# Performance work log

Hardware: AMD Instinct MI355X
Metric: run time of the kernel (lower is better)

Reference implementation:

```python
import jax, jax.numpy as jnp
import numpy as np

B, T, LD, HD, NH, NL = 8, 16, 256, 512, 8, 6
N = 65           # num_patches + 1 tokens per frame from encoder
AED = 64         # action_embed_dim
NDA = 11         # num_discrete_actions
MLP = 4 * HD


def _ln(x, g, b, eps=1e-5):
    m = jnp.mean(x, -1, keepdims=True)
    v = jnp.mean((x - m) ** 2, -1, keepdims=True)
    return (x - m) / jnp.sqrt(v + eps) * g + b


def setup_inputs() -> dict:
    key = jax.random.key(0)
    ks = iter(jax.random.split(key, 48))
    def nrm(shape):
        return jax.random.normal(next(ks), shape, jnp.float32) * 0.02
    inp = {
        'z_sequence': jax.random.normal(next(ks), (B, T, N, LD), jnp.float32),
        'continuous_actions': jax.random.normal(next(ks), (B, T, 2), jnp.float32),
        'discrete_actions': jax.random.randint(next(ks), (B, T), 0, NDA),
        'w_de': nrm((NDA, AED)),
        'w_cp': nrm((2, AED)), 'b_cp': jnp.zeros((AED,), jnp.float32),
        'w_ap': nrm((2 * AED, HD)), 'b_ap': jnp.zeros((HD,), jnp.float32),
        'w_tp': nrm((LD, HD)), 'b_tp': jnp.zeros((HD,), jnp.float32),
        'w_te': nrm((64, HD)),
        'ln1_g': jnp.ones((NL, HD), jnp.float32), 'ln1_b': jnp.zeros((NL, HD), jnp.float32),
        'wq': nrm((NL, HD, HD)), 'bq': jnp.zeros((NL, HD), jnp.float32),
        'wk': nrm((NL, HD, HD)), 'bk': jnp.zeros((NL, HD), jnp.float32),
        'wv': nrm((NL, HD, HD)), 'bv': jnp.zeros((NL, HD), jnp.float32),
        'wo': nrm((NL, HD, HD)), 'bo': jnp.zeros((NL, HD), jnp.float32),
        'ln2_g': jnp.ones((NL, HD), jnp.float32), 'ln2_b': jnp.zeros((NL, HD), jnp.float32),
        'w1': nrm((NL, HD, MLP)), 'b1': jnp.zeros((NL, MLP), jnp.float32),
        'w2': nrm((NL, MLP, HD)), 'b2': jnp.zeros((NL, HD), jnp.float32),
        'norm_g': jnp.ones((HD,), jnp.float32), 'norm_b': jnp.zeros((HD,), jnp.float32),
        'w_out': nrm((HD, LD)), 'b_out': jnp.zeros((LD,), jnp.float32),
        'residual_weight': jnp.float32(0.5),
    }
    return inp


def reference(z_sequence, continuous_actions, discrete_actions,
              w_de, w_cp, b_cp, w_ap, b_ap, w_tp, b_tp, w_te,
              ln1_g, ln1_b, wq, bq, wk, bk, wv, bv, wo, bo,
              ln2_g, ln2_b, w1, b1, w2, b2,
              norm_g, norm_b, w_out, b_out, residual_weight):
    Bq, Tq, Nq, Dq = z_sequence.shape
    hd = HD // NH
    scale = hd ** -0.5
    # --- per-timestep action + patch token embedding (vectorized over T) ---
    de = w_de[discrete_actions]                          # (B,T,AED)
    ce = continuous_actions @ w_cp + b_cp                # (B,T,AED)
    ac = jnp.concatenate([de, ce], -1)                   # (B,T,2*AED)
    at = (ac @ w_ap + b_ap)[:, :, None, :]               # (B,T,1,HD) action token
    pt = z_sequence @ w_tp + b_tp                        # (B,T,N,HD)
    te = w_te[:Tq][None, :, None, :]                     # (1,T,1,HD) time embedding
    x = jnp.concatenate([at + te, pt + te], axis=2)      # (B,T,1+N,HD) interleaved
    S = Tq * (Nq + 1)
    x = x.reshape(Bq, S, HD)
    # --- block-causal mask: True = cannot attend ---
    ts = jnp.repeat(jnp.arange(Tq), Nq + 1)
    mask = ts[None, :] > ts[:, None]                     # (S,S)

    def body(h, p):
        g1, be1, Wq, Bq_, Wk, Bk_, Wv, Bv_, Wo, Bo_, g2, be2, W1, B1, W2, B2 = p
        y = _ln(h, g1, be1)
        q = (y @ Wq + Bq_).reshape(Bq, S, NH, hd)
        k = (y @ Wk + Bk_).reshape(Bq, S, NH, hd)
        v = (y @ Wv + Bv_).reshape(Bq, S, NH, hd)
        sc = jnp.einsum('bqhd,bkhd->bhqk', q, k) * scale
        sc = jnp.where(mask[None, None], -jnp.inf, sc)
        a = jax.nn.softmax(sc, axis=-1)
        o = jnp.einsum('bhqk,bkhd->bqhd', a, v).reshape(Bq, S, HD)
        h = h + o @ Wo + Bo_
        y = _ln(h, g2, be2)
        h = h + jax.nn.gelu(y @ W1 + B1, approximate=False) @ W2 + B2
        return h, None

    x, _ = jax.lax.scan(body, x, (ln1_g, ln1_b, wq, bq, wk, bk, wv, bv, wo, bo,
                                  ln2_g, ln2_b, w1, b1, w2, b2))
    x = _ln(x, norm_g, norm_b)
    patch_out = x.reshape(Bq, Tq, Nq + 1, HD)[:, :, 1:, :] @ w_out + b_out
    alpha = jax.nn.sigmoid(residual_weight)
    return z_sequence + alpha * patch_out
```

## Files before the change

kernel.cpp:

```cpp
#include <hip/hip_runtime.h>
#include <hip/hip_bf16.h>
#include <cmath>

typedef __attribute__((ext_vector_type(8)))  __bf16 bf16x8;
typedef __attribute__((ext_vector_type(4)))  float  f32x4;
typedef __attribute__((ext_vector_type(16))) float  f32x16;
typedef const __attribute__((address_space(1))) void* as1cv;
typedef __attribute__((address_space(3))) void*       as3v;

#define GBAR()  asm volatile("s_barrier" ::: "memory")
#define VMW0()  asm volatile("s_waitcnt vmcnt(0)" ::: "memory")

static constexpr int BB = 8, TT = 16, NN = 65, LD = 256, HD = 512, NH = 8, NL = 6;
static constexpr int SS    = TT * (NN + 1);
static constexpr int ROWS  = BB * SS;
static constexpr int PROWS = BB * TT * NN;
static constexpr int MLPD  = 2048;

__global__ void transpose_cast(const float* __restrict__ in, __bf16* __restrict__ out,
                               int R, int C, size_t ibs, size_t obs)
{
  __shared__ float t[32][33];
  in  += ibs * blockIdx.z;
  out += obs * blockIdx.z;
  int bx = blockIdx.x * 32, by = blockIdx.y * 32;
  #pragma unroll
  for (int i = threadIdx.y; i < 32; i += 8)
    t[i][threadIdx.x] = in[(size_t)(by + i) * C + bx + threadIdx.x];
  __syncthreads();
  #pragma unroll
  for (int i = threadIdx.y; i < 32; i += 8)
    out[(size_t)(bx + i) * R + by + threadIdx.x] = (__bf16)t[threadIdx.x][i];
}

__global__ __launch_bounds__(256) void cast_bf16(const float* __restrict__ in,
                                                 __bf16* __restrict__ out)
{
  int i = (blockIdx.x * 256 + threadIdx.x) * 8;
  float4 a = *(const float4*)(in + i);
  float4 b = *(const float4*)(in + i + 4);
  bf16x8 o;
  o[0]=(__bf16)a.x; o[1]=(__bf16)a.y; o[2]=(__bf16)a.z; o[3]=(__bf16)a.w;
  o[4]=(__bf16)b.x; o[5]=(__bf16)b.y; o[6]=(__bf16)b.z; o[7]=(__bf16)b.w;
  *(bf16x8*)(out + i) = o;
}

__global__ void build_bqkv(const float* __restrict__ bq, const float* __restrict__ bk,
                           const float* __restrict__ bv, float* __restrict__ out)
{
  int i = blockIdx.x * 256 + threadIdx.x;
  int L = i / 1536, c = i % 1536;
  float v = (c < 512) ? bq[L*512 + c] : (c < 1024 ? bk[L*512 + c - 512] : bv[L*512 + c - 1024]);
  out[i] = v;
}

template<int FLAGS>
__global__ __launch_bounds__(256)
void gemm_bt(const __bf16* __restrict__ A, const __bf16* __restrict__ Bt,
             const float* __restrict__ bias, const float* __restrict__ resid,
             float* __restrict__ outF, __bf16* __restrict__ outB, __bf16* __restrict__ outB2,
             int M, int N, int K)
{
  __shared__ __bf16 As[64 * 64];
  __shared__ __bf16 Bs[128 * 64];
  const int tid = threadIdx.x;
  const int lane = tid & 63, w = tid >> 6;
  const int g = lane >> 4, cl = lane & 15;
  const int wr = w >> 1, wc = w & 1;
  const int gx = gridDim.x, nwg = gx * gridDim.y;
  const int orig = blockIdx.y * gx + blockIdx.x;
  const int q8 = nwg >> 3, r8 = nwg & 7;
  const int xcd = orig & 7, off = orig >> 3;
  const int tile = (xcd < r8 ? xcd * (q8 + 1) : r8 * (q8 + 1) + (xcd - r8) * q8) + off;
  const int tm = (tile / gx) * 64, tn = (tile % gx) * 128;

  f32x4 acc[2][4];
  const f32x4 zero4 = {0.f, 0.f, 0.f, 0.f};
  #pragma unroll
  for (int m = 0; m < 2; m++)
    #pragma unroll
    for (int n = 0; n < 4; n++) acc[m][n] = zero4;

  const int nk = K >> 6;
  for (int kt = 0; kt < nk; ++kt) {
    __syncthreads();
    const __bf16* Ag = A  + (size_t)tm * K + kt * 64;
    const __bf16* Bg = Bt + (size_t)tn * K + kt * 64;
    #pragma unroll
    for (int p = 0; p < 2; p++) {
      int c = p * 256 + tid;
      int row = c >> 3, j = c & 7;
      int jj = j ^ (row & 7);
      const __bf16* sa = Ag + (size_t)row * K + jj * 8;
      __builtin_amdgcn_global_load_lds((as1cv)sa, (as3v)&As[(p * 4 + w) * 512], 16, 0, 0);
    }
    #pragma unroll
    for (int p = 0; p < 4; p++) {
      int c = p * 256 + tid;
      int row = c >> 3, j = c & 7;
      int jj = j ^ (row & 7);
      const __bf16* sb = Bg + (size_t)row * K + jj * 8;
      __builtin_amdgcn_global_load_lds((as1cv)sb, (as3v)&Bs[(p * 4 + w) * 512], 16, 0, 0);
    }
    __syncthreads();
    #pragma unroll
    for (int kk = 0; kk < 2; kk++) {
      bf16x8 af[2], bfr[4];
      #pragma unroll
      for (int m = 0; m < 2; m++) {
        int row = wr * 32 + m * 16 + cl;
        af[m] = *(const bf16x8*)&As[row * 64 + ((kk * 4 + g) ^ (row & 7)) * 8];
      }
      #pragma unroll
      for (int n = 0; n < 4; n++) {
        int row = wc * 64 + n * 16 + cl;
        bfr[n] = *(const bf16x8*)&Bs[row * 64 + ((kk * 4 + g) ^ (row & 7)) * 8];
      }
      #pragma unroll
      for (int m = 0; m < 2; m++)
        #pragma unroll
        for (int n = 0; n < 4; n++)
          acc[m][n] = __builtin_amdgcn_mfma_f32_16x16x32_bf16(af[m], bfr[n], acc[m][n], 0, 0, 0);
    }
  }
  float bv[4];
  #pragma unroll
  for (int n = 0; n < 4; n++) bv[n] = bias[tn + wc * 64 + n * 16 + cl];
  #pragma unroll
  for (int m = 0; m < 2; m++) {
    int Rb = tm + wr * 32 + m * 16 + g * 4;
    #pragma unroll
    for (int i = 0; i < 4; i++) {
      int R = Rb + i;
      #pragma unroll
      for (int n = 0; n < 4; n++) {
        int C = tn + wc * 64 + n * 16 + cl;
        float v = acc[m][n][i] + bv[n];
        if (FLAGS & 1) v = 0.5f * v * (1.f + erff(v * 0.70710678118f));
        if (FLAGS & 2) v += resid[(size_t)R * N + C];
        if (FLAGS & 8) outF[(size_t)R * N + C] = v;
        if (FLAGS & 4) outB[(size_t)R * N + C] = (__bf16)v;
        if (FLAGS & 32) {
          if (C < 1024) {
            outB[(size_t)R * 1024 + C] = (__bf16)v;
          } else {
            int bb2 = R / SS, s2 = R % SS;
            int cc = C - 1024, hh = cc >> 6, dd = cc & 63;
            outB2[((size_t)((bb2 * NH + hh) * 64 + dd)) * SS + s2] = (__bf16)v;
          }
        }
      }
    }
  }
}

__global__ __launch_bounds__(256) void ln_bf16(const float* __restrict__ in,
    const float* __restrict__ gam, const float* __restrict__ bet, __bf16* __restrict__ out)
{
  int w = threadIdx.x >> 6, l = threadIdx.x & 63;
  size_t row = (size_t)blockIdx.x * 4 + w;
  const float4* x4 = (const float4*)(in + row * HD);
  float4 v0 = x4[l], v1 = x4[l + 64];
  float s  = v0.x + v0.y + v0.z + v0.w + v1.x + v1.y + v1.z + v1.w;
  float q2 = v0.x*v0.x + v0.y*v0.y + v0.z*v0.z + v0.w*v0.w
           + v1.x*v1.x + v1.y*v1.y + v1.z*v1.z + v1.w*v1.w;
  #pragma unroll
  for (int m = 1; m < 64; m <<= 1) { s += __shfl_xor(s, m); q2 += __shfl_xor(q2, m); }
  float mean = s * (1.f / HD);
  float rstd = rsqrtf(q2 * (1.f / HD) - mean * mean + 1e-5f);
  int c0 = l * 4, c1 = 256 + l * 4;
  float4 g0 = *(const float4*)(gam + c0), g1 = *(const float4*)(gam + c1);
  float4 e0 = *(const float4*)(bet + c0), e1 = *(const float4*)(bet + c1);
  __bf16* o = out + row * HD;
  o[c0+0] = (__bf16)((v0.x-mean)*rstd*g0.x + e0.x);
  o[c0+1] = (__bf16)((v0.y-mean)*rstd*g0.y + e0.y);
  o[c0+2] = (__bf16)((v0.z-mean)*rstd*g0.z + e0.z);
  o[c0+3] = (__bf16)((v0.w-mean)*rstd*g0.w + e0.w);
  o[c1+0] = (__bf16)((v1.x-mean)*rstd*g1.x + e1.x);
  o[c1+1] = (__bf16)((v1.y-mean)*rstd*g1.y + e1.y);
  o[c1+2] = (__bf16)((v1.z-mean)*rstd*g1.z + e1.z);
  o[c1+3] = (__bf16)((v1.w-mean)*rstd*g1.w + e1.w);
}

__global__ __launch_bounds__(64) void act_embed(const float* __restrict__ cont,
    const int* __restrict__ disc, const float* __restrict__ w_de,
    const float* __restrict__ w_cp, const float* __restrict__ b_cp,
    const float* __restrict__ w_ap, const float* __restrict__ b_ap,
    const float* __restrict__ w_te, float* __restrict__ x)
{
  int t = blockIdx.x, b = blockIdx.y, l = threadIdx.x;
  int da = disc[b * TT + t];
  float c0 = cont[(b * TT + t) * 2], c1 = cont[(b * TT + t) * 2 + 1];
  int c = l * 8;
  float accv[8];
  #pragma unroll
  for (int j = 0; j < 8; j++) accv[j] = b_ap[c + j];
  for (int i = 0; i < 64; i++) {
    float ai = w_de[da * 64 + i];
    #pragma unroll
    for (int j = 0; j < 8; j++) accv[j] += ai * w_ap[i * HD + c + j];
  }
  for (int i = 0; i < 64; i++) {
    float ce = c0 * w_cp[i] + c1 * w_cp[64 + i] + b_cp[i];
    #pragma unroll
    for (int j = 0; j < 8; j++) accv[j] += ce * w_ap[(64 + i) * HD + c + j];
  }
  #pragma unroll
  for (int j = 0; j < 8; j++)
    x[((size_t)(b * SS) + t * 66) * HD + c + j] = accv[j] + w_te[t * HD + c + j];
}

__global__ __launch_bounds__(256) void assemble_patch(const float* __restrict__ pt,
    const float* __restrict__ te, float* __restrict__ x)
{
  int idx = (blockIdx.x * 256 + threadIdx.x) * 4;
  int c = idx & (HD - 1);
  int r = idx >> 9;
  int n = r % NN; int bt = r / NN; int t = bt & (TT - 1); int bb = bt >> 4;
  float4 v  = *(const float4*)(pt + idx);
  float4 tv = *(const float4*)(te + t * HD + c);
  v.x += tv.x; v.y += tv.y; v.z += tv.z; v.w += tv.w;
  *(float4*)(x + ((size_t)(bb * SS + t * 66 + 1 + n)) * HD + c) = v;
}

__device__ inline unsigned pkbf(float lo, float hi2) {
  unsigned short a = __builtin_bit_cast(unsigned short, (__bf16)lo);
  unsigned short b = __builtin_bit_cast(unsigned short, (__bf16)hi2);
  return (unsigned)a | ((unsigned)b << 16);
}

__global__ __launch_bounds__(256) void attn_fwd(const __bf16* __restrict__ qk,
    const __bf16* __restrict__ vT, __bf16* __restrict__ o)
{
  const int tid = threadIdx.x;
  const int w = tid >> 6, lane = tid & 63;
  const int h = blockIdx.y, b = blockIdx.z;
  const int l31 = lane & 31, hi = lane >> 5;
  const int qt = blockIdx.x * 4 + w;
  const bool qv = qt <= 32;
  const int q = qv ? qt * 32 + l31 : 0;
  const int kend = (q / 66 + 1) * 66;

  __shared__ __attribute__((aligned(16))) __bf16 Ks[2][64][64];
  __shared__ __attribute__((aligned(16))) __bf16 Vs[2][64][64];
  __shared__ float red[4][32];

  const int qtmax = min(blockIdx.x * 4 + 3, 32);
  const int nkv_b = (((qtmax * 32 + 31) / 66 + 1) * 66 + 63) >> 6;
  const int nkv_w = qv ? ((((qt * 32 + 31) / 66 + 1) * 66 + 63) >> 6) : 0;

  bf16x8 qf[4];
  const __bf16* qbase = qk + (size_t)(b * SS + q) * 1024 + h * 64 + hi * 8;
  #pragma unroll
  for (int s = 0; s < 4; s++) qf[s] = *(const bf16x8*)(qbase + s * 16);

  const f32x16 z16 = {0,0,0,0,0,0,0,0,0,0,0,0,0,0,0,0};
  f32x16 accA = z16, accB = z16;
  float m = -1e30f, lsum = 0.f;

  auto stage = [&](int buf, int kb) {
    const int K0 = kb * 64;
    #pragma unroll
    for (int p2 = 0; p2 < 2; p2++) {
      int c = p2 * 256 + tid;
      int row = c >> 3, j = c & 7;
      int jj = j ^ (row & 7);
      const __bf16* sk = qk + (size_t)(b * SS + min(K0 + row, SS - 1)) * 1024 + 512
                            + h * 64 + jj * 8;
      __builtin_amdgcn_global_load_lds((as1cv)sk,
          (as3v)(&Ks[buf][0][0] + (p2 * 4 + w) * 512), 16, 0, 0);
      const __bf16* sv = vT + (size_t)((b * NH + h) * 64 + row) * SS
                            + min(K0 + jj * 8, SS - 8);
      __builtin_amdgcn_global_load_lds((as1cv)sv,
          (as3v)(&Vs[buf][0][0] + (p2 * 4 + w) * 512), 16, 0, 0);
    }
  };

  stage(0, 0);
  VMW0();
  GBAR();

  int buf = 0;
  for (int kb = 0; kb < nkv_b; ++kb) {
    if (kb + 1 < nkv_b) stage(buf ^ 1, kb + 1);
    if (qv && kb < nkv_w) {
      const int K0 = kb * 64;
      bf16x8 kfa[4], kfb[4], vfa[4], vfb[4];
      #pragma unroll
      for (int s = 0; s < 4; s++) {
        int ch = ((s * 2 + hi) ^ (l31 & 7)) * 8;
        kfa[s] = *(const bf16x8*)&Ks[buf][l31][ch];
        kfb[s] = *(const bf16x8*)&Ks[buf][32 + l31][ch];
        vfa[s] = *(const bf16x8*)&Vs[buf][l31][ch];
        vfb[s] = *(const bf16x8*)&Vs[buf][32 + l31][ch];
      }
      f32x16 st0 = z16, st1 = z16;
      st0 = __builtin_amdgcn_mfma_f32_32x32x16_bf16(kfa[0], qf[0], st0, 0, 0, 0);
      st0 = __builtin_amdgcn_mfma_f32_32x32x16_bf16(kfa[1], qf[1], st0, 0, 0, 0);
      st0 = __builtin_amdgcn_mfma_f32_32x32x16_bf16(kfa[2], qf[2], st0, 0, 0, 0);
      st0 = __builtin_amdgcn_mfma_f32_32x32x16_bf16(kfa[3], qf[3], st0, 0, 0, 0);
      st1 = __builtin_amdgcn_mfma_f32_32x32x16_bf16(kfb[0], qf[0], st1, 0, 0, 0);
      st1 = __builtin_amdgcn_mfma_f32_32x32x16_bf16(kfb[1], qf[1], st1, 0, 0, 0);
      st1 = __builtin_amdgcn_mfma_f32_32x32x16_bf16(kfb[2], qf[2], st1, 0, 0, 0);
      st1 = __builtin_amdgcn_mfma_f32_32x32x16_bf16(kfb[3], qf[3], st1, 0, 0, 0);

      float p0[16], p1[16];
      #pragma unroll
      for (int r = 0; r < 16; r++) {
        int cr = (r & 3) + 8 * (r >> 2) + 4 * hi;
        p0[r] = (K0 + cr < kend)      ? st0[r] * 0.125f : -1e30f;
        p1[r] = (K0 + 32 + cr < kend) ? st1[r] * 0.125f : -1e30f;
      }
      float mx = fmaxf(fmaxf(fmaxf(p0[0],p0[1]),fmaxf(p0[2],p0[3])),
                       fmaxf(fmaxf(p0[4],p0[5]),fmaxf(p0[6],p0[7])));
      mx = fmaxf(mx, fmaxf(fmaxf(fmaxf(p0[8],p0[9]),fmaxf(p0[10],p0[11])),
                           fmaxf(fmaxf(p0[12],p0[13]),fmaxf(p0[14],p0[15]))));
      mx = fmaxf(mx, fmaxf(fmaxf(fmaxf(p1[0],p1[1]),fmaxf(p1[2],p1[3])),
                           fmaxf(fmaxf(p1[4],p1[5]),fmaxf(p1[6],p1[7]))));
      mx = fmaxf(mx, fmaxf(fmaxf(fmaxf(p1[8],p1[9]),fmaxf(p1[10],p1[11])),
                           fmaxf(fmaxf(p1[12],p1[13]),fmaxf(p1[14],p1[15]))));
      mx = fmaxf(mx, __shfl_xor(mx, 32));
      if (__any(mx > m + 8.f)) {
        float nm = fmaxf(m, mx);
        float alp = __expf(m - nm);
        m = nm; lsum *= alp;
        if (lane < 32) red[w][lane] = alp;
        asm volatile("s_waitcnt lgkmcnt(0)" ::: "memory");
        float4 a0 = *(const float4*)&red[w][hi * 4];
        float4 a1 = *(const float4*)&red[w][hi * 4 + 8];
        float4 a2 = *(const float4*)&red[w][hi * 4 + 16];
        float4 a3 = *(const float4*)&red[w][hi * 4 + 24];
        float afv[16] = {a0.x,a0.y,a0.z,a0.w, a1.x,a1.y,a1.z,a1.w,
                         a2.x,a2.y,a2.z,a2.w, a3.x,a3.y,a3.z,a3.w};
        #pragma unroll
        for (int r = 0; r < 16; r++) { accA[r] *= afv[r]; accB[r] *= afv[r]; }
      }
      #pragma unroll
      for (int r = 0; r < 16; r++) { p0[r] = __expf(p0[r] - m); p1[r] = __expf(p1[r] - m); }
      float rs = (((p0[0]+p0[1])+(p0[2]+p0[3])) + ((p0[4]+p0[5])+(p0[6]+p0[7])))
               + (((p0[8]+p0[9])+(p0[10]+p0[11])) + ((p0[12]+p0[13])+(p0[14]+p0[15])))
               + (((p1[0]+p1[1])+(p1[2]+p1[3])) + ((p1[4]+p1[5])+(p1[6]+p1[7])))
               + (((p1[8]+p1[9])+(p1[10]+p1[11])) + ((p1[12]+p1[13])+(p1[14]+p1[15])));
      rs += __shfl_xor(rs, 32);
      lsum += rs;
      union { unsigned u[4]; bf16x8 v; } af00, af10, af01, af11;
      {
        unsigned a0p = pkbf(p0[0], p0[1]),  a1p = pkbf(p0[2], p0[3]);
        unsigned a2p = pkbf(p0[4], p0[5]),  a3p = pkbf(p0[6], p0[7]);
        unsigned b0p = pkbf(p0[8], p0[9]),  b1p = pkbf(p0[10], p0[11]);
        unsigned b2p = pkbf(p0[12], p0[13]), b3p = pkbf(p0[14], p0[15]);
        unsigned s0 = __shfl_xor(a0p, 32), s1 = __shfl_xor(a1p, 32);
        unsigned s2 = __shfl_xor(a2p, 32), s3 = __shfl_xor(a3p, 32);
        unsigned t0 = __shfl_xor(b0p, 32), t1 = __shfl_xor(b1p, 32);
        unsigned t2 = __shfl_xor(b2p, 32), t3 = __shfl_xor(b3p, 32);
        af00.u[0] = hi ? s2 : a0p;  af00.u[1] = hi ? s3 : a1p;
        af00.u[2] = hi ? a2p : s0;  af00.u[3] = hi ? a3p : s1;
        af10.u[0] = hi ? t2 : b0p;  af10.u[1] = hi ? t3 : b1p;
        af10.u[2] = hi ? b2p : t0;  af10.u[3] = hi ? b3p : t1;
      }
      {
        unsigned a0p = pkbf(p1[0], p1[1]),  a1p = pkbf(p1[2], p1[3]);
        unsigned a2p = pkbf(p1[4], p1[5]),  a3p = pkbf(p1[6], p1[7]);
        unsigned b0p = pkbf(p1[8], p1[9]),  b1p = pkbf(p1[10], p1[11]);
        unsigned b2p = pkbf(p1[12], p1[13]), b3p = pkbf(p1[14], p1[15]);
        unsigned s0 = __shfl_xor(a0p, 32), s1 = __shfl_xor(a1p, 32);
        unsigned s2 = __shfl_xor(a2p, 32), s3 = __shfl_xor(a3p, 32);
        unsigned t0 = __shfl_xor(b0p, 32), t1 = __shfl_xor(b1p, 32);
        unsigned t2 = __shfl_xor(b2p, 32), t3 = __shfl_xor(b3p, 32);
        af01.u[0] = hi ? s2 : a0p;  af01.u[1] = hi ? s3 : a1p;
        af01.u[2] = hi ? a2p : s0;  af01.u[3] = hi ? a3p : s1;
        af11.u[0] = hi ? t2 : b0p;  af11.u[1] = hi ? t3 : b1p;
        af11.u[2] = hi ? b2p : t0;  af11.u[3] = hi ? b3p : t1;
      }
      accA = __builtin_amdgcn_mfma_f32_32x32x16_bf16(af00.v, vfa[0], accA, 0, 0, 0);
      accA = __builtin_amdgcn_mfma_f32_32x32x16_bf16(af10.v, vfa[1], accA, 0, 0, 0);
      accA = __builtin_amdgcn_mfma_f32_32x32x16_bf16(af01.v, vfa[2], accA, 0, 0, 0);
      accA = __builtin_amdgcn_mfma_f32_32x32x16_bf16(af11.v, vfa[3], accA, 0, 0, 0);
      accB = __builtin_amdgcn_mfma_f32_32x32x16_bf16(af00.v, vfb[0], accB, 0, 0, 0);
      accB = __builtin_amdgcn_mfma_f32_32x32x16_bf16(af10.v, vfb[1], accB, 0, 0, 0);
      accB = __builtin_amdgcn_mfma_f32_32x32x16_bf16(af01.v, vfb[2], accB, 0, 0, 0);
      accB = __builtin_amdgcn_mfma_f32_32x32x16_bf16(af11.v, vfb[3], accB, 0, 0, 0);
    }
    VMW0();
    GBAR();
    buf ^= 1;
  }

  if (qv) {
    if (lane < 32) red[w][lane] = 1.f / lsum;
    asm volatile("s_waitcnt lgkmcnt(0)" ::: "memory");
    float4 i0 = *(const float4*)&red[w][hi * 4];
    float4 i1 = *(const float4*)&red[w][hi * 4 + 8];
    float4 i2 = *(const float4*)&red[w][hi * 4 + 16];
    float4 i3 = *(const float4*)&red[w][hi * 4 + 24];
    float iv[16] = {i0.x,i0.y,i0.z,i0.w, i1.x,i1.y,i1.z,i1.w,
                    i2.x,i2.y,i2.z,i2.w, i3.x,i3.y,i3.z,i3.w};
    __bf16* obase = o + (size_t)(b * SS + qt * 32) * HD + h * 64 + l31;
    #pragma unroll
    for (int r = 0; r < 16; r++) {
      int qrow = (r & 3) + 8 * (r >> 2) + 4 * hi;
      obase[(size_t)qrow * HD]      = (__bf16)(accA[r] * iv[r]);
      obase[(size_t)qrow * HD + 32] = (__bf16)(accB[r] * iv[r]);
    }
  }
}

__global__ __launch_bounds__(256) void final_add(const float* __restrict__ z,
    const float* __restrict__ po, const float* __restrict__ rw, float* __restrict__ out)
{
  int idx = (blockIdx.x * 256 + threadIdx.x) * 4;
  int ld = idx & (LD - 1);
  int r = idx >> 8;
  int n = r % NN; int bt = r / NN; int t = bt & (TT - 1); int bb = bt >> 4;
  float alpha = 1.f / (1.f + __expf(-rw[0]));
  float4 zv = *(const float4*)(z + idx);
  float4 pv = *(const float4*)(po + ((size_t)(bb * SS + t * 66 + 1 + n)) * LD + ld);
  float4 ov;
  ov.x = zv.x + alpha * pv.x; ov.y = zv.y + alpha * pv.y;
  ov.z = zv.z + alpha * pv.z; ov.w = zv.w + alpha * pv.w;
  *(float4*)(out + idx) = ov;
}

extern "C" void kernel_launch(void* const* d_in, const int* in_sizes, int n_in,
                              void* d_out, int out_size, void* d_ws, size_t ws_size,
                              hipStream_t stream)
{
  const float* z    = (const float*)d_in[0];
  const float* cont = (const float*)d_in[1];
  const int*   disc = (const int*)d_in[2];
  const float* w_de = (const float*)d_in[3];
  const float* w_cp = (const float*)d_in[4];
  const float* b_cp = (const float*)d_in[5];
  const float* w_ap = (const float*)d_in[6];
  const float* b_ap = (const float*)d_in[7];
  const float* w_tp = (const float*)d_in[8];
  const float* b_tp = (const float*)d_in[9];
  const float* w_te = (const float*)d_in[10];
  const float* ln1g = (const float*)d_in[11];
  const float* ln1b = (const float*)d_in[12];
  const float* wq   = (const float*)d_in[13];
  const float* bq   = (const float*)d_in[14];
  const float* wk   = (const float*)d_in[15];
  const float* bk   = (const float*)d_in[16];
  const float* wv   = (const float*)d_in[17];
  const float* bv   = (const float*)d_in[18];
  const float* wo   = (const float*)d_in[19];
  const float* bo   = (const float*)d_in[20];
  const float* ln2g = (const float*)d_in[21];
  const float* ln2b = (const float*)d_in[22];
  const float* w1   = (const float*)d_in[23];
  const float* b1   = (const float*)d_in[24];
  const float* w2   = (const float*)d_in[25];
  const float* b2   = (const float*)d_in[26];
  const float* nog  = (const float*)d_in[27];
  const float* nob  = (const float*)d_in[28];
  const float* wout = (const float*)d_in[29];
  const float* bout = (const float*)d_in[30];
  const float* rw   = (const float*)d_in[31];
  float* out = (float*)d_out;

  char* p = (char*)d_ws;
  auto alloc = [&](size_t bytes) -> char* {
    char* r = p; p += (bytes + 255) & ~(size_t)255; return r;
  };
  __bf16* wqkvt = (__bf16*)alloc((size_t)NL * 1536 * 512 * 2);
  __bf16* wot_  = (__bf16*)alloc((size_t)NL * 512 * 512 * 2);
  __bf16* w1t   = (__bf16*)alloc((size_t)NL * 512 * 2048 * 2);
  __bf16* w2t   = (__bf16*)alloc((size_t)NL * 512 * 2048 * 2);
  __bf16* wtpt  = (__bf16*)alloc((size_t)512 * 256 * 2);
  __bf16* woutt = (__bf16*)alloc((size_t)256 * 512 * 2);
  float*  bqkv  = (float*)alloc((size_t)NL * 1536 * 4);
  __bf16* zbf   = (__bf16*)alloc((size_t)PROWS * LD * 2);
  float*  x     = (float*)alloc((size_t)ROWS * HD * 4);
  __bf16* y     = (__bf16*)alloc((size_t)ROWS * HD * 2);
  __bf16* qkb   = (__bf16*)alloc((size_t)ROWS * 1024 * 2);
  __bf16* vtb   = (__bf16*)alloc((size_t)ROWS * HD * 2);
  __bf16* ob    = (__bf16*)alloc((size_t)ROWS * HD * 2);
  __bf16* mid   = (__bf16*)alloc((size_t)ROWS * MLPD * 2);
  float*  ptb   = (float*)alloc((size_t)PROWS * HD * 4);
  (void)in_sizes; (void)n_in; (void)out_size; (void)ws_size;

  dim3 tb(32, 8);
  transpose_cast<<<dim3(16, 16, 6), tb, 0, stream>>>(wq, wqkvt,          512,  512,  262144, 786432);
  transpose_cast<<<dim3(16, 16, 6), tb, 0, stream>>>(wk, wqkvt + 262144, 512,  512,  262144, 786432);
  transpose_cast<<<dim3(16, 16, 6), tb, 0, stream>>>(wv, wqkvt + 524288, 512,  512,  262144, 786432);
  transpose_cast<<<dim3(16, 16, 6), tb, 0, stream>>>(wo, wot_,           512,  512,  262144, 262144);
  transpose_cast<<<dim3(64, 16, 6), tb, 0, stream>>>(w1, w1t,            512,  2048, 1048576, 1048576);
  transpose_cast<<<dim3(16, 64, 6), tb, 0, stream>>>(w2, w2t,            2048, 512,  1048576, 1048576);
  transpose_cast<<<dim3(16, 8, 1),  tb, 0, stream>>>(w_tp, wtpt,         256,  512,  0, 0);
  transpose_cast<<<dim3(8, 16, 1),  tb, 0, stream>>>(wout, woutt,        512,  256,  0, 0);
  build_bqkv<<<36, 256, 0, stream>>>(bq, bk, bv, bqkv);
  cast_bf16<<<(PROWS * LD) / 2048, 256, 0, stream>>>(z, zbf);

  gemm_bt<8><<<dim3(4, PROWS / 64), 256, 0, stream>>>(zbf, wtpt, b_tp, nullptr, ptb, nullptr,
                                                      nullptr, PROWS, 512, 256);
  act_embed<<<dim3(16, 8), 64, 0, stream>>>(cont, disc, w_de, w_cp, b_cp, w_ap, b_ap, w_te, x);
  assemble_patch<<<(PROWS * HD) / 1024, 256, 0, stream>>>(ptb, w_te, x);

  for (int L = 0; L < NL; ++L) {
    ln_bf16<<<ROWS / 4, 256, 0, stream>>>(x, ln1g + L*HD, ln1b + L*HD, y);
    gemm_bt<32><<<dim3(12, ROWS / 64), 256, 0, stream>>>(y, wqkvt + (size_t)L*786432,
                                                         bqkv + L*1536, nullptr, nullptr,
                                                         qkb, vtb, ROWS, 1536, 512);
    attn_fwd<<<dim3(9, NH, BB), 256, 0, stream>>>(qkb, vtb, ob);
    gemm_bt<10><<<dim3(4, ROWS / 64), 256, 0, stream>>>(ob, wot_ + (size_t)L*262144, bo + L*HD,
                                                        x, x, nullptr, nullptr, ROWS, 512, 512);
    ln_bf16<<<ROWS / 4, 256, 0, stream>>>(x, ln2g + L*HD, ln2b + L*HD, y);
    gemm_bt<5><<<dim3(16, ROWS / 64), 256, 0, stream>>>(y, w1t + (size_t)L*1048576, b1 + L*MLPD,
                                                        nullptr, nullptr, mid, nullptr,
                                                        ROWS, 2048, 512);
    gemm_bt<10><<<dim3(4, ROWS / 64), 256, 0, stream>>>(mid, w2t + (size_t)L*1048576, b2 + L*HD,
                                                        x, x, nullptr, nullptr, ROWS, 512, 2048);
  }
  ln_bf16<<<ROWS / 4, 256, 0, stream>>>(x, nog, nob, y);
  gemm_bt<8><<<dim3(2, ROWS / 64), 256, 0, stream>>>(y, woutt, bout, nullptr, ptb, nullptr,
                                                     nullptr, ROWS, 256, 512);
  final_add<<<(PROWS * LD) / 1024, 256, 0, stream>>>(z, ptb, rw, out);
}
```

Baseline: 1.093 ms.

## Add 64x64-tile GEMM for N=512 projections and XCD-aware attention block remap

Adds a gemm_n64 kernel with 64x64 output tiles, 16x16x32 MFMAs, swizzled LDS and an XCD-aware tile remapping. It replaces the 64x128 gemm_bt for the patch projection, the attention output projection, the MLP down projection and the final output projection, doubling the number of workgroups for these narrow-N GEMMs to fill more CUs. The attention kernel switches to a 1D grid whose block index is remapped so that blocks sharing a batch and head land on the same XCD, which should improve L2 reuse of K/V. The new GEMM has no double buffering, and smaller tiles mean less data reuse per load.

```diff
diff --git a/kernel.cpp b/kernel.cpp
--- a/kernel.cpp
+++ b/kernel.cpp
@@ -154,6 +154,91 @@
   }
 }
 
+template<int FLAGS>
+__global__ __launch_bounds__(256)
+void gemm_n64(const __bf16* __restrict__ A, const __bf16* __restrict__ Bt,
+              const float* __restrict__ bias, const float* __restrict__ resid,
+              float* __restrict__ outF, __bf16* __restrict__ outB,
+              int M, int N, int K)
+{
+  __shared__ __bf16 As[64 * 64];
+  __shared__ __bf16 Bs[64 * 64];
+  const int tid = threadIdx.x;
+  const int lane = tid & 63, w = tid >> 6;
+  const int g = lane >> 4, cl = lane & 15;
+  const int wr = w >> 1, wc = w & 1;
+  const int gx = gridDim.x, nwg = gx * gridDim.y;
+  const int orig = blockIdx.y * gx + blockIdx.x;
+  const int q8 = nwg >> 3, r8 = nwg & 7;
+  const int xcd = orig & 7, off = orig >> 3;
+  const int tile = (xcd < r8 ? xcd * (q8 + 1) : r8 * (q8 + 1) + (xcd - r8) * q8) + off;
+  const int tm = (tile / gx) * 64, tn = (tile % gx) * 64;
+
+  f32x4 acc[2][2];
+  const f32x4 zero4 = {0.f, 0.f, 0.f, 0.f};
+  #pragma unroll
+  for (int m = 0; m < 2; m++)
+    #pragma unroll
+    for (int n = 0; n < 2; n++) acc[m][n] = zero4;
+
+  const int nk = K >> 6;
+  for (int kt = 0; kt < nk; ++kt) {
+    __syncthreads();
+    const __bf16* Ag = A  + (size_t)tm * K + kt * 64;
+    const __bf16* Bg = Bt + (size_t)tn * K + kt * 64;
+    #pragma unroll
+    for (int p = 0; p < 2; p++) {
+      int c = p * 256 + tid;
+      int row = c >> 3, j = c & 7;
+      int jj = j ^ (row & 7);
+      const __bf16* sa = Ag + (size_t)row * K + jj * 8;
+      const __bf16* sb = Bg + (size_t)row * K + jj * 8;
+      __builtin_amdgcn_global_load_lds((as1cv)sa, (as3v)&As[(p * 4 + w) * 512], 16, 0, 0);
+      __builtin_amdgcn_global_load_lds((as1cv)sb, (as3v)&Bs[(p * 4 + w) * 512], 16, 0, 0);
+    }
+    __syncthreads();
+    #pragma unroll
+    for (int kk = 0; kk < 2; kk++) {
+      bf16x8 af[2], bfr[2];
+      #pragma unroll
+      for (int m = 0; m < 2; m++) {
+        int row = wr * 32 + m * 16 + cl;
+        af[m] = *(const bf16x8*)&As[row * 64 + ((kk * 4 + g) ^ (row & 7)) * 8];
+      }
+      #pragma unroll
+      for (int n = 0; n < 2; n++) {
+        int row = wc * 32 + n * 16 + cl;
+        bfr[n] = *(const bf16x8*)&Bs[row * 64 + ((kk * 4 + g) ^ (row & 7)) * 8];
+      }
+      #pragma unroll
+      for (int m = 0; m < 2; m++)
+        #pragma unroll
+        for (int n = 0; n < 2; n++)
+          acc[m][n] = __builtin_amdgcn_mfma_f32_16x16x32_bf16(af[m], bfr[n], acc[m][n], 0, 0, 0);
+    }
+  }
+  float bv[2];
+  #pragma unroll
+  for (int n = 0; n < 2; n++) bv[n] = bias[tn + wc * 32 + n * 16 + cl];
+  #pragma unroll
+  for (int m = 0; m < 2; m++) {
+    int Rb = tm + wr * 32 + m * 16 + g * 4;
+    #pragma unroll
+    for (int i = 0; i < 4; i++) {
+      int R = Rb + i;
+      #pragma unroll
+      for (int n = 0; n < 2; n++) {
+        int C = tn + wc * 32 + n * 16 + cl;
+        float v = acc[m][n][i] + bv[n];
+        if (FLAGS & 1) v = 0.5f * v * (1.f + erff(v * 0.70710678118f));
+        if (FLAGS & 2) v += resid[(size_t)R * N + C];
+        if (FLAGS & 8) outF[(size_t)R * N + C] = v;
+        if (FLAGS & 4) outB[(size_t)R * N + C] = (__bf16)v;
+      }
+    }
+  }
+}
+
 __global__ __launch_bounds__(256) void ln_bf16(const float* __restrict__ in,
     const float* __restrict__ gam, const float* __restrict__ bet, __bf16* __restrict__ out)
 {
@@ -234,9 +319,12 @@
 {
   const int tid = threadIdx.x;
   const int w = tid >> 6, lane = tid & 63;
-  const int h = blockIdx.y, b = blockIdx.z;
+  const int lin = (blockIdx.x & 7) * 72 + (blockIdx.x >> 3);
+  const int qb = lin % 9;
+  const int h  = (lin / 9) & 7;
+  const int b  = lin / 72;
   const int l31 = lane & 31, hi = lane >> 5;
-  const int qt = blockIdx.x * 4 + w;
+  const int qt = qb * 4 + w;
   const bool qv = qt <= 32;
   const int q = qv ? qt * 32 + l31 : 0;
   const int kend = (q / 66 + 1) * 66;
@@ -245,7 +333,7 @@
   __shared__ __attribute__((aligned(16))) __bf16 Vs[2][64][64];
   __shared__ float red[4][32];
 
-  const int qtmax = min(blockIdx.x * 4 + 3, 32);
+  const int qtmax = min(qb * 4 + 3, 32);
   const int nkv_b = (((qtmax * 32 + 31) / 66 + 1) * 66 + 63) >> 6;
   const int nkv_w = qv ? ((((qt * 32 + 31) / 66 + 1) * 66 + 63) >> 6) : 0;
 
@@ -492,8 +580,8 @@
   build_bqkv<<<36, 256, 0, stream>>>(bq, bk, bv, bqkv);
   cast_bf16<<<(PROWS * LD) / 2048, 256, 0, stream>>>(z, zbf);
 
-  gemm_bt<8><<<dim3(4, PROWS / 64), 256, 0, stream>>>(zbf, wtpt, b_tp, nullptr, ptb, nullptr,
-                                                      nullptr, PROWS, 512, 256);
+  gemm_n64<8><<<dim3(8, PROWS / 64), 256, 0, stream>>>(zbf, wtpt, b_tp, nullptr, ptb, nullptr,
+                                                       PROWS, 512, 256);
   act_embed<<<dim3(16, 8), 64, 0, stream>>>(cont, disc, w_de, w_cp, b_cp, w_ap, b_ap, w_te, x);
   assemble_patch<<<(PROWS * HD) / 1024, 256, 0, stream>>>(ptb, w_te, x);
 
@@ -502,18 +590,18 @@
     gemm_bt<32><<<dim3(12, ROWS / 64), 256, 0, stream>>>(y, wqkvt + (size_t)L*786432,
                                                          bqkv + L*1536, nullptr, nullptr,
                                                          qkb, vtb, ROWS, 1536, 512);
-    attn_fwd<<<dim3(9, NH, BB), 256, 0, stream>>>(qkb, vtb, ob);
-    gemm_bt<10><<<dim3(4, ROWS / 64), 256, 0, stream>>>(ob, wot_ + (size_t)L*262144, bo + L*HD,
-                                                        x, x, nullptr, nullptr, ROWS, 512, 512);
+    attn_fwd<<<576, 256, 0, stream>>>(qkb, vtb, ob);
+    gemm_n64<10><<<dim3(8, ROWS / 64), 256, 0, stream>>>(ob, wot_ + (size_t)L*262144, bo + L*HD,
+                                                         x, x, nullptr, ROWS, 512, 512);
     ln_bf16<<<ROWS / 4, 256, 0, stream>>>(x, ln2g + L*HD, ln2b + L*HD, y);
     gemm_bt<5><<<dim3(16, ROWS / 64), 256, 0, stream>>>(y, w1t + (size_t)L*1048576, b1 + L*MLPD,
                                                         nullptr, nullptr, mid, nullptr,
                                                         ROWS, 2048, 512);
-    gemm_bt<10><<<dim3(4, ROWS / 64), 256, 0, stream>>>(mid, w2t + (size_t)L*1048576, b2 + L*HD,
-                                                        x, x, nullptr, nullptr, ROWS, 512, 2048);
+    gemm_n64<10><<<dim3(8, ROWS / 64), 256, 0, stream>>>(mid, w2t + (size_t)L*1048576, b2 + L*HD,
+                                                         x, x, nullptr, ROWS, 512, 2048);
   }
   ln_bf16<<<ROWS / 4, 256, 0, stream>>>(x, nog, nob, y);
-  gemm_bt<8><<<dim3(2, ROWS / 64), 256, 0, stream>>>(y, woutt, bout, nullptr, ptb, nullptr,
-                                                     nullptr, ROWS, 256, 512);
+  gemm_n64<8><<<dim3(4, ROWS / 64), 256, 0, stream>>>(y, woutt, bout, nullptr, ptb, nullptr,
+                                                      ROWS, 256, 512);
   final_add<<<(PROWS * LD) / 1024, 256, 0, stream>>>(z, ptb, rw, out);
 }
```

Result: faster. 1.054 ms (-3.5%).
